# Performance work log

Hardware: AMD Instinct MI355X
Metric: run time of the kernel (lower is better)

## Reference

```python
import jax, jax.numpy as jnp
import numpy as np

B, S, D = 2, 2048, 4096
H, ROT = 16, 64
HD = D // H  # 256


def rotate_every_two(x):
    # x: (..., d) with d even; interleave (-x_odd, x_even)
    x1 = x[..., ::2]
    x2 = x[..., 1::2]
    return jnp.stack((-x2, x1), axis=-1).reshape(x.shape)


def setup_inputs() -> dict:
    key = jax.random.key(0)
    ks = jax.random.split(key, 8)
    hidden_states = jax.random.normal(ks[0], (B, S, D), dtype=jnp.float32)
    # GPT-J style repeat-interleaved sin/cos over rotary_dim, broadcast over heads
    inv_freq = 1.0 / (10000.0 ** (jnp.arange(0, ROT, 2, dtype=jnp.float32) / ROT))
    t = jnp.arange(S, dtype=jnp.float32)
    freqs = jnp.einsum('s,f->sf', t, inv_freq)                    # (S, ROT/2)
    freqs = jnp.repeat(freqs, 2, axis=-1)                         # (S, ROT)
    sin = jnp.sin(freqs)[None, :, None, :]                        # (1, S, 1, ROT)
    cos = jnp.cos(freqs)[None, :, None, :]
    scale = 0.02
    Wq = jax.random.normal(ks[1], (D, D), dtype=jnp.float32) * scale
    Wk = jax.random.normal(ks[2], (D, D), dtype=jnp.float32) * scale
    Wv = jax.random.normal(ks[3], (D, D), dtype=jnp.float32) * scale
    Wo = jax.random.normal(ks[4], (D, D), dtype=jnp.float32) * scale
    return {"hidden_states": hidden_states, "sin": sin, "cos": cos,
            "Wq": Wq, "Wk": Wk, "Wv": Wv, "Wo": Wo}


def reference(hidden_states, sin, cos, Wq, Wk, Wv, Wo):
    b, s, d = hidden_states.shape
    # projections (nn.Linear, no bias): y = x @ W.T
    q = (hidden_states @ Wq.T).reshape(b, s, H, HD)
    k = (hidden_states @ Wk.T).reshape(b, s, H, HD)
    v = (hidden_states @ Wv.T).reshape(b, s, H, HD)

    def rope(x):
        x_rot, x_pass = x[..., :ROT], x[..., ROT:]
        x_rot = x_rot * cos + rotate_every_two(x_rot) * sin
        return jnp.concatenate([x_rot, x_pass], axis=-1)

    q = rope(q).transpose(0, 2, 1, 3)  # (B, H, S, HD)
    k = rope(k).transpose(0, 2, 1, 3)
    v = v.transpose(0, 2, 1, 3)

    inv_scale = 1.0 / np.sqrt(HD).astype(np.float32)
    scores = jnp.einsum('bhqd,bhkd->bhqk', q, k) * inv_scale      # (B, H, S, S)
    # scaled_masked_triangular_softmax == causal masked softmax
    causal = jnp.tril(jnp.ones((s, s), dtype=bool))
    scores = jnp.where(causal[None, None], scores, jnp.finfo(scores.dtype).min)
    attn = jax.nn.softmax(scores, axis=-1)
    out = jnp.einsum('bhqk,bhkd->bhqd', attn, v)                  # (B, H, S, HD)
    out = out.transpose(0, 2, 1, 3).reshape(b, s, d)              # merge heads
    return out @ Wo.T
```

## Files before the change

kernel.cpp:

```cpp
#include <hip/hip_runtime.h>
#include <cstdint>
#include <cstddef>

#define TB 2
#define TS 2048
#define TD 4096
#define TH 16
#define THD 256
#define TROT 64
#define TM (TB*TS)

typedef __attribute__((ext_vector_type(8))) short bf16x8;
typedef __attribute__((ext_vector_type(4))) float f32x4;

#define LGKM0  asm volatile("s_waitcnt lgkmcnt(0)" ::: "memory")
#define VMCNT8 asm volatile("s_waitcnt vmcnt(8)" ::: "memory")
#define VMCNT4 asm volatile("s_waitcnt vmcnt(4)" ::: "memory")
#define VMCNT0 asm volatile("s_waitcnt vmcnt(0)" ::: "memory")
#define SBAR   __builtin_amdgcn_s_barrier()
#define SCHED0 __builtin_amdgcn_sched_barrier(0)
#define PRIO1  __builtin_amdgcn_s_setprio(1)
#define PRIO0  __builtin_amdgcn_s_setprio(0)

#if __has_builtin(__builtin_amdgcn_exp2f)
#define EXP2(x) __builtin_amdgcn_exp2f(x)
#else
#define EXP2(x) exp2f(x)
#endif

__device__ __forceinline__ unsigned short f2bf(float f) {
  union { float f; unsigned u; } v; v.f = f;
  return (unsigned short)((v.u + 0x7fffu + ((v.u >> 16) & 1u)) >> 16);
}

__device__ __forceinline__ void gld16(const void* g, void* l) {
  __builtin_amdgcn_global_load_lds(
      (const __attribute__((address_space(1))) unsigned int*)g,
      (__attribute__((address_space(3))) unsigned int*)l, 16, 0, 0);
}

__global__ __launch_bounds__(256) void k_cvt5(
    const float* __restrict__ s0, const float* __restrict__ s1,
    const float* __restrict__ s2, const float* __restrict__ s3,
    const float* __restrict__ s4, unsigned short* __restrict__ dst) {
  int i = blockIdx.x * 256 + threadIdx.x;
  int tsel = i >> 22, il = i & 4194303;
  const float* s = tsel == 0 ? s0 : tsel == 1 ? s1 : tsel == 2 ? s2 : tsel == 3 ? s3 : s4;
  float4 v = reinterpret_cast<const float4*>(s)[il];
  ushort4 o;
  o.x = f2bf(v.x); o.y = f2bf(v.y); o.z = f2bf(v.z); o.w = f2bf(v.w);
  *reinterpret_cast<ushort4*>(dst + (size_t)i * 4) = o;
}

#define GSTG(SBUF, SAB, SHALF, SKOFS) { \
    const unsigned short* _s = (SAB) ? srcB : srcA; \
    const int _b = (SBUF)*32768 + (SAB)*16384 + (SHALF)*8192; \
    gld16(_s + (size_t)(SHALF)*128*TD + (SKOFS) + roff[0], &lds[_b + t*8]); \
    gld16(_s + (size_t)(SHALF)*128*TD + (SKOFS) + roff[1], &lds[_b + (512+t)*8]); }

#define GLD_AF(DST, BUF, QA) { \
    _Pragma("unroll") for (int m = 0; m < 4; ++m) \
    _Pragma("unroll") for (int kk = 0; kk < 2; ++kk) \
      DST[m][kk] = *(const bf16x8*)&lds[(BUF)*32768 + (QA)*8192 + ((wm*4+m)*2+kk)*512 + llo]; }

#define GLD_BQ(DST, BUF, QB) { \
    _Pragma("unroll") for (int n = 0; n < 2; ++n) \
    _Pragma("unroll") for (int kk = 0; kk < 2; ++kk) \
      DST[n][kk] = *(const bf16x8*)&lds[(BUF)*32768 + 16384 + (QB)*8192 + ((wn*2+n)*2+kk)*512 + llo]; }

#define GMF(AF, BQ, QA, QB) { \
    _Pragma("unroll") for (int kk = 0; kk < 2; ++kk) \
    _Pragma("unroll") for (int m = 0; m < 4; ++m) \
    _Pragma("unroll") for (int n = 0; n < 2; ++n) \
      acc[QA][QB][m][n] = __builtin_amdgcn_mfma_f32_16x16x32_bf16( \
          AF[m][kk], BQ[n][kk], acc[QA][QB][m][n], 0,0,0); }

#define GEMM_MAIN_LOOP \
  GSTG(0,0,0, 0);  SCHED0; \
  GSTG(0,1,0, 0);  SCHED0; \
  GSTG(0,0,1, 0);  SCHED0; \
  GSTG(0,1,1, 0);  SCHED0; \
  GSTG(1,0,0, 64); SCHED0; \
  GSTG(1,1,0, 64); SCHED0; \
  VMCNT4; SBAR; SCHED0; \
  for (int i2 = 0; i2 < NT/2; ++i2) { \
    const int k1c = (2*i2+1) * 64; \
    const int k0n = (2*i2+2 < NT ? 2*i2+2 : NT-1) * 64; \
    const int k1n = (2*i2+3 < NT ? 2*i2+3 : NT-1) * 64; \
     \
    GLD_AF(afP, 0, 0); GLD_BQ(bqP, 0, 0); \
    GSTG(1,0,1, k1c); \
    LGKM0; SCHED0; \
    PRIO1; GLD_BQ(bqQ, 0, 1); GMF(afP, bqP, 0, 0); PRIO0; SCHED0; \
     \
    GSTG(1,1,1, k1c); \
    LGKM0; SCHED0; \
    PRIO1; GLD_AF(afQ, 0, 1); GMF(afP, bqQ, 0, 1); PRIO0; \
    SBAR; SCHED0; \
     \
    GSTG(0,0,0, k0n); \
    LGKM0; SCHED0; \
    PRIO1; GMF(afQ, bqP, 1, 0); PRIO0; SCHED0; \
     \
    GSTG(0,1,0, k0n); \
    VMCNT4; SBAR; \
    LGKM0; SCHED0; \
    PRIO1; GMF(afQ, bqQ, 1, 1); PRIO0; SCHED0; \
     \
    GLD_AF(afP, 1, 0); GLD_BQ(bqP, 1, 0); \
    GSTG(0,0,1, k0n); \
    LGKM0; SCHED0; \
    PRIO1; GLD_BQ(bqQ, 1, 1); GMF(afP, bqP, 0, 0); PRIO0; SCHED0; \
     \
    GSTG(0,1,1, k0n); \
    LGKM0; SCHED0; \
    PRIO1; GLD_AF(afQ, 1, 1); GMF(afP, bqQ, 0, 1); PRIO0; \
    SBAR; SCHED0; \
     \
    GSTG(1,0,0, k1n); \
    LGKM0; SCHED0; \
    PRIO1; GMF(afQ, bqP, 1, 0); PRIO0; SCHED0; \
     \
    GSTG(1,1,0, k1n); \
    VMCNT4; SBAR; \
    LGKM0; SCHED0; \
    PRIO1; GMF(afQ, bqQ, 1, 1); PRIO0; SCHED0; \
  }

#define GEMM_PREAMBLE \
  const int K = TD; \
  const int t = threadIdx.x; \
  const int w = t >> 6, l = t & 63, lr = l & 15, lh = l >> 4; \
  const int wm = w >> 2, wn = w & 3; \
  const int llo = lr * 32 + ((lh ^ ((lr >> 1) & 3)) * 8); \
  int roff[2]; \
  _Pragma("unroll") \
  for (int it = 0; it < 2; ++it) { \
    int c = it * 512 + t; \
    int rl = (c >> 2) & 15; \
    roff[it] = (16 * (c >> 7) + rl) * K + ((c >> 6) & 1) * 32 + ((c & 3) ^ ((rl >> 1) & 3)) * 8; \
  } \
  f32x4 acc[2][2][4][2]; \
  _Pragma("unroll") \
  for (int qa = 0; qa < 2; ++qa) \
  _Pragma("unroll") \
    for (int qb = 0; qb < 2; ++qb) \
  _Pragma("unroll") \
      for (int m = 0; m < 4; ++m) \
  _Pragma("unroll") \
        for (int n = 0; n < 2; ++n) acc[qa][qb][m][n] = 0.f; \
  bf16x8 afP[4][2], afQ[4][2], bqP[2][2], bqQ[2][2]; \
  const int NT = K / 64;

__global__ __launch_bounds__(512, 1) void k_gqkv(
    const unsigned short* __restrict__ A, const unsigned short* __restrict__ W,
    unsigned short* __restrict__ Qo, unsigned short* __restrict__ Ko,
    unsigned short* __restrict__ Vo,
    const float* __restrict__ sinp, const float* __restrict__ cosp)
{
  extern __shared__ unsigned short lds[];
  const int id = blockIdx.x;
  const int xcd = id & 7, kk_ = id >> 3;
  const int m0 = ((xcd & 1) * 8 + kk_ / 12) * 256;
  const int n0 = ((xcd >> 1) * 12 + kk_ % 12) * 256;

  GEMM_PREAMBLE
  const unsigned short* srcA = A + (size_t)m0 * K;
  const unsigned short* srcB = W + (size_t)n0 * K;

  GEMM_MAIN_LOOP

  VMCNT0;
  const int tsel = n0 >> 12;
  if (tsel == 2) {
    SBAR;
    const int n0v = n0 - 8192;
    const int b = m0 >> 11, sbase = m0 & (TS - 1);
#pragma unroll
    for (int qb = 0; qb < 2; ++qb)
#pragma unroll
      for (int n = 0; n < 2; ++n) {
        __syncthreads();
#pragma unroll
        for (int qa = 0; qa < 2; ++qa)
#pragma unroll
          for (int m = 0; m < 4; ++m) {
            int lcol = wn * 16 + lr;
            int srow = qa * 128 + wm * 64 + m * 16 + lh * 4;
            ushort4 o;
            o.x = f2bf(acc[qa][qb][m][n][0]); o.y = f2bf(acc[qa][qb][m][n][1]);
            o.z = f2bf(acc[qa][qb][m][n][2]); o.w = f2bf(acc[qa][qb][m][n][3]);
            *(ushort4*)&lds[lcol * 268 + srow] = o;
          }
        __syncthreads();
#pragma unroll
        for (int rr = 0; rr < 4; ++rr) {
          int idx = rr * 512 + t;
          int dl = idx >> 5, sc = (idx & 31) * 8;
          uint4 v = *(const uint4*)&lds[dl * 268 + sc];
          int d = n0v + qb * 128 + (dl >> 4) * 32 + n * 16 + (dl & 15);
          *(uint4*)(Vo + ((size_t)((b * TH + (d >> 8)) * THD + (d & 255))) * TS + sbase + sc) = v;
        }
      }
  } else {
    unsigned short* outp = tsel ? Ko : Qo;
    const int nbase = n0 & 4095;
#pragma unroll
    for (int qa = 0; qa < 2; ++qa)
#pragma unroll
      for (int qb = 0; qb < 2; ++qb)
#pragma unroll
        for (int m = 0; m < 4; ++m)
#pragma unroll
          for (int n = 0; n < 2; ++n)
#pragma unroll
            for (int r = 0; r < 4; ++r) {
              int row = m0 + qa * 128 + wm * 64 + m * 16 + lh * 4 + r;
              int col = nbase + qb * 128 + wn * 32 + n * 16 + lr;
              float x = acc[qa][qb][m][n][r];
              float part = __shfl_xor(x, 1, 64);
              int s = row & (TS - 1), b = row >> 11;
              int h = col >> 8, d = col & 255;
              float val = x;
              if (d < TROT) {
                float cc = cosp[s * TROT + d], ss = sinp[s * TROT + d];
                val = x * cc + ((d & 1) ? part : -part) * ss;
              }
              outp[((size_t)(b * TH + h) * TS + s) * THD + d] = f2bf(val);
            }
  }
}

__global__ __launch_bounds__(512, 1) void k_gout(
    const unsigned short* __restrict__ A, const unsigned short* __restrict__ W,
    float* __restrict__ out)
{
  extern __shared__ unsigned short lds[];
  const int id = blockIdx.x;
  const int xcd = id & 7, kk_ = id >> 3;
  const int m0 = ((xcd >> 1) * 4 + (kk_ >> 3)) * 256;
  const int n0 = ((xcd & 1) * 8 + (kk_ & 7)) * 256;

  GEMM_PREAMBLE
  const unsigned short* srcA = A + (size_t)m0 * K;
  const unsigned short* srcB = W + (size_t)n0 * K;

  GEMM_MAIN_LOOP

  VMCNT0;
#pragma unroll
  for (int qa = 0; qa < 2; ++qa)
#pragma unroll
    for (int qb = 0; qb < 2; ++qb)
#pragma unroll
      for (int m = 0; m < 4; ++m)
#pragma unroll
        for (int n = 0; n < 2; ++n)
#pragma unroll
          for (int r = 0; r < 4; ++r) {
            int row = m0 + qa * 128 + wm * 64 + m * 16 + lh * 4 + r;
            int col = n0 + qb * 128 + wn * 32 + n * 16 + lr;
            out[(size_t)row * TD + col] = acc[qa][qb][m][n][r];
          }
}

__global__ __launch_bounds__(256, 2) void k_fattn(
    const unsigned short* __restrict__ Qt, const unsigned short* __restrict__ Kt,
    const unsigned short* __restrict__ Vt, unsigned short* __restrict__ O)
{
  extern __shared__ unsigned short sh[];
  const int t = threadIdx.x, w = t >> 6, l = t & 63, lr = l & 15, lh = l >> 4;
  const int bh = blockIdx.x;
  const int qb = (gridDim.y - 1) - blockIdx.y;
  const int q0 = qb * 64;
  const int jmax = qb;
  const float SC = 0.0625f * 1.44269504f;

  const unsigned short* kbase = Kt + (size_t)bh * TS * THD;
  const unsigned short* vbase = Vt + (size_t)bh * THD * TS;

  const int llo = lr * 32 + ((lh ^ ((lr >> 1) & 3)) * 8);

  int koff[8], voff[8];
#pragma unroll
  for (int it = 0; it < 8; ++it) {
    int c = it * 256 + t;
    int row = (c >> 2) & 15;
    int scc = (c & 3) ^ ((row >> 1) & 3);
    koff[it] = (((c >> 9) & 3) * 16 + row) * THD + ((c >> 6) & 7) * 32 + scc * 8;
    voff[it] = (((c >> 6) & 15) * 16 + row) * TS + ((c >> 10) & 1) * 32 + scc * 8;
  }

  bf16x8 qf[8];
  const unsigned short* qp = Qt + ((size_t)bh * TS + q0 + w * 16 + lr) * THD;
#pragma unroll
  for (int kk = 0; kk < 8; ++kk) qf[kk] = *(const bf16x8*)(qp + kk * 32 + lh * 8);

  f32x4 oacc[16];
#pragma unroll
  for (int i = 0; i < 16; ++i) oacc[i] = 0.f;
  float mrow[4] = {-__builtin_inff(), -__builtin_inff(), -__builtin_inff(), -__builtin_inff()};
  float lrow[4] = {0.f, 0.f, 0.f, 0.f};

#pragma unroll
  for (int it = 0; it < 8; ++it) gld16(kbase + koff[it], &sh[(it*256 + t) * 8]);
#pragma unroll
  for (int it = 0; it < 8; ++it) gld16(vbase + voff[it], &sh[16384 + (it*256 + t) * 8]);

  for (int j = 0; j <= jmax; ++j) {
    const bool nx = (j < jmax);
    VMCNT8; SBAR; SCHED0;

    f32x4 sacc[4];
#pragma unroll
    for (int nt = 0; nt < 4; ++nt) sacc[nt] = 0.f;
    PRIO1;
#pragma unroll
    for (int kk = 0; kk < 8; ++kk)
#pragma unroll
      for (int nt = 0; nt < 4; ++nt) {
        bf16x8 kf = *(const bf16x8*)&sh[(nt*8 + kk)*512 + llo];
        sacc[nt] = __builtin_amdgcn_mfma_f32_16x16x32_bf16(qf[kk], kf, sacc[nt], 0, 0, 0);
      }
    PRIO0;
    LGKM0; SBAR; SCHED0;
    if (nx) {
      const unsigned short* kj = kbase + (size_t)(j + 1) * 64 * THD;
#pragma unroll
      for (int it = 0; it < 8; ++it) gld16(kj + koff[it], &sh[(it*256 + t) * 8]);
    }

    float p[4][4];
    const int qrow0 = q0 + w * 16 + lh * 4;
    if (j == jmax) {
#pragma unroll
      for (int nt = 0; nt < 4; ++nt) {
        int kpos = j * 64 + nt * 16 + lr;
#pragma unroll
        for (int r = 0; r < 4; ++r) {
          float sv = sacc[nt][r] * SC;
          if (kpos > qrow0 + r) sv = -__builtin_inff();
          p[nt][r] = sv;
        }
      }
    } else {
#pragma unroll
      for (int nt = 0; nt < 4; ++nt)
#pragma unroll
        for (int r = 0; r < 4; ++r)
          p[nt][r] = sacc[nt][r] * SC;
    }
    float lmax[4];
#pragma unroll
    for (int r = 0; r < 4; ++r)
      lmax[r] = fmaxf(fmaxf(p[0][r], p[1][r]), fmaxf(p[2][r], p[3][r]));
    float g = fmaxf(fmaxf(lmax[0] - mrow[0], lmax[1] - mrow[1]),
                    fmaxf(lmax[2] - mrow[2], lmax[3] - mrow[3]));
    if (__any(g > 11.5416f)) {
      float tmax[4] = {lmax[0], lmax[1], lmax[2], lmax[3]};
#pragma unroll
      for (int off = 1; off < 16; off <<= 1)
#pragma unroll
        for (int r = 0; r < 4; ++r) tmax[r] = fmaxf(tmax[r], __shfl_xor(tmax[r], off, 64));
      float alpha[4];
#pragma unroll
      for (int r = 0; r < 4; ++r) {
        float mn = fmaxf(mrow[r], tmax[r]);
        alpha[r] = EXP2(mrow[r] - mn);
        mrow[r] = mn;
        lrow[r] *= alpha[r];
      }
#pragma unroll
      for (int i = 0; i < 16; ++i)
#pragma unroll
        for (int r = 0; r < 4; ++r) oacc[i][r] *= alpha[r];
    }
#pragma unroll
    for (int r = 0; r < 4; ++r) {
      float pe0 = EXP2(p[0][r] - mrow[r]);
      float pe1 = EXP2(p[1][r] - mrow[r]);
      float pe2 = EXP2(p[2][r] - mrow[r]);
      float pe3 = EXP2(p[3][r] - mrow[r]);
      p[0][r] = pe0; p[1][r] = pe1; p[2][r] = pe2; p[3][r] = pe3;
      lrow[r] += (pe0 + pe1) + (pe2 + pe3);
    }

    const int wb = 32768 + w * 1152;
#pragma unroll
    for (int nt = 0; nt < 4; ++nt)
#pragma unroll
      for (int r = 0; r < 4; ++r)
        sh[wb + (lh*4 + r)*72 + nt*16 + lr] = f2bf(p[nt][r]);
    bf16x8 pfr0 = *(const bf16x8*)&sh[wb + lr*72 + lh*8];
    bf16x8 pfr1 = *(const bf16x8*)&sh[wb + lr*72 + 32 + lh*8];

    if (nx) { VMCNT8; } else { VMCNT0; }
    SBAR; SCHED0;
    PRIO1;
#pragma unroll
    for (int dt = 0; dt < 16; ++dt) {
      bf16x8 vf = *(const bf16x8*)&sh[16384 + dt*512 + llo];
      oacc[dt] = __builtin_amdgcn_mfma_f32_16x16x32_bf16(pfr0, vf, oacc[dt], 0, 0, 0);
    }
#pragma unroll
    for (int dt = 0; dt < 16; ++dt) {
      bf16x8 vf = *(const bf16x8*)&sh[16384 + (16 + dt)*512 + llo];
      oacc[dt] = __builtin_amdgcn_mfma_f32_16x16x32_bf16(pfr1, vf, oacc[dt], 0, 0, 0);
    }
    PRIO0;
    LGKM0; SBAR; SCHED0;
    if (nx) {
      const unsigned short* vj = vbase + (size_t)(j + 1) * 64;
#pragma unroll
      for (int it = 0; it < 8; ++it) gld16(vj + voff[it], &sh[16384 + (it*256 + t) * 8]);
    }
  }

#pragma unroll
  for (int off = 1; off < 16; off <<= 1)
#pragma unroll
    for (int r = 0; r < 4; ++r) lrow[r] += __shfl_xor(lrow[r], off, 64);

  const int b = bh >> 4, h = bh & 15;
  float inv[4];
#pragma unroll
  for (int r = 0; r < 4; ++r) inv[r] = 1.f / lrow[r];
#pragma unroll
  for (int dt = 0; dt < 16; ++dt)
#pragma unroll
    for (int r = 0; r < 4; ++r) {
      int s = q0 + w * 16 + lh * 4 + r;
      O[((size_t)(b * TS + s) * TH + h) * THD + dt * 16 + lr] = f2bf(oacc[dt][r] * inv[r]);
    }
}

extern "C" void kernel_launch(void* const* d_in, const int* in_sizes, int n_in,
                              void* d_out, int out_size, void* d_ws, size_t ws_size,
                              hipStream_t stream) {
  const float* hs   = (const float*)d_in[0];
  const float* sinp = (const float*)d_in[1];
  const float* cosp = (const float*)d_in[2];
  const float* Wq   = (const float*)d_in[3];
  const float* Wk   = (const float*)d_in[4];
  const float* Wv   = (const float*)d_in[5];
  const float* Wo   = (const float*)d_in[6];

  const size_t NE = (size_t)TM * TD;
  const size_t BYTES = NE * 2;
  char* ws = (char*)d_ws;
  unsigned short* hsb = (unsigned short*)(ws + 0*BYTES);
  unsigned short* Wqb = (unsigned short*)(ws + 1*BYTES);
  unsigned short* Wob = (unsigned short*)(ws + 4*BYTES);
  unsigned short* Qt  = (unsigned short*)(ws + 5*BYTES);
  unsigned short* Ktb = (unsigned short*)(ws + 6*BYTES);
  unsigned short* Vtb = (unsigned short*)(ws + 7*BYTES);
  unsigned short* Ob  = (unsigned short*)(ws + 8*BYTES);

  k_cvt5<<<81920, 256, 0, stream>>>(hs, Wq, Wk, Wv, Wo, hsb);

  k_gqkv<<<768, 512, 131072, stream>>>(hsb, Wqb, Qt, Ktb, Vtb, sinp, cosp);

  k_fattn<<<dim3(TB*TH, TS/64), 256, 74752, stream>>>(Qt, Ktb, Vtb, Ob);

  k_gout<<<256, 512, 131072, stream>>>(Ob, Wob, (float*)d_out);
}
```

Measured before the change: 672.5 us.

## Enlarge attention query tile to 128 rows with 8 waves sharing K/V tiles

The flash-attention kernel now handles 128 query rows per block with 512 threads (8 waves), so each K/V tile loaded into shared memory serves twice as many query rows and global K/V traffic halves. Query blocks are reordered so the longest causal rows launch first. Waves whose rows lie entirely above a key tile skip that tile's compute, and only tiles straddling the diagonal apply the mask. The P staging buffer now uses an XOR swizzle instead of padding. In exchange, idle waves wait at barriers on skipped tiles, and the grid drops to 512 blocks with more LDS per block, which may reduce occupancy and load balance.

```diff
diff --git a/kernel.cpp b/kernel.cpp
--- a/kernel.cpp
+++ b/kernel.cpp
@@ -264,16 +264,17 @@
           }
 }
 
-__global__ __launch_bounds__(256, 2) void k_fattn(
+__global__ __launch_bounds__(512, 2) void k_fattn(
     const unsigned short* __restrict__ Qt, const unsigned short* __restrict__ Kt,
     const unsigned short* __restrict__ Vt, unsigned short* __restrict__ O)
 {
   extern __shared__ unsigned short sh[];
   const int t = threadIdx.x, w = t >> 6, l = t & 63, lr = l & 15, lh = l >> 4;
   const int bh = blockIdx.x;
-  const int qb = (gridDim.y - 1) - blockIdx.y;
-  const int q0 = qb * 64;
-  const int jmax = qb;
+  const int y = blockIdx.y;
+  const int qb = (y < 8) ? (15 - y) : (y - 8);
+  const int q0 = qb * 128;
+  const int jmax = 2 * qb + 1;
   const float SC = 0.0625f * 1.44269504f;
 
   const unsigned short* kbase = Kt + (size_t)bh * TS * THD;
@@ -281,10 +282,10 @@
 
   const int llo = lr * 32 + ((lh ^ ((lr >> 1) & 3)) * 8);
 
-  int koff[8], voff[8];
-#pragma unroll
-  for (int it = 0; it < 8; ++it) {
-    int c = it * 256 + t;
+  int koff[4], voff[4];
+#pragma unroll
+  for (int it = 0; it < 4; ++it) {
+    int c = it * 512 + t;
     int row = (c >> 2) & 15;
     int scc = (c & 3) ^ ((row >> 1) & 3);
     koff[it] = (((c >> 9) & 3) * 16 + row) * THD + ((c >> 6) & 7) * 32 + scc * 8;
@@ -303,118 +304,133 @@
   float lrow[4] = {0.f, 0.f, 0.f, 0.f};
 
 #pragma unroll
-  for (int it = 0; it < 8; ++it) gld16(kbase + koff[it], &sh[(it*256 + t) * 8]);
-#pragma unroll
-  for (int it = 0; it < 8; ++it) gld16(vbase + voff[it], &sh[16384 + (it*256 + t) * 8]);
+  for (int it = 0; it < 4; ++it) gld16(kbase + koff[it], &sh[(it*512 + t) * 8]);
+#pragma unroll
+  for (int it = 0; it < 4; ++it) gld16(vbase + voff[it], &sh[16384 + (it*512 + t) * 8]);
+
+  const int qw = q0 + w * 16;
+  const int psb = 32768 + w * 1024;
 
   for (int j = 0; j <= jmax; ++j) {
     const bool nx = (j < jmax);
-    VMCNT8; SBAR; SCHED0;
+    const bool active = (j * 64) <= (qw + 15);
+    const bool diag   = (j * 64 + 63) > qw;
+    VMCNT4; SBAR; SCHED0;
 
     f32x4 sacc[4];
 #pragma unroll
     for (int nt = 0; nt < 4; ++nt) sacc[nt] = 0.f;
-    PRIO1;
-#pragma unroll
-    for (int kk = 0; kk < 8; ++kk)
-#pragma unroll
-      for (int nt = 0; nt < 4; ++nt) {
-        bf16x8 kf = *(const bf16x8*)&sh[(nt*8 + kk)*512 + llo];
-        sacc[nt] = __builtin_amdgcn_mfma_f32_16x16x32_bf16(qf[kk], kf, sacc[nt], 0, 0, 0);
-      }
-    PRIO0;
-    LGKM0; SBAR; SCHED0;
+    if (active) {
+      PRIO1;
+#pragma unroll
+      for (int kk = 0; kk < 8; ++kk)
+#pragma unroll
+        for (int nt = 0; nt < 4; ++nt) {
+          bf16x8 kf = *(const bf16x8*)&sh[(nt*8 + kk)*512 + llo];
+          sacc[nt] = __builtin_amdgcn_mfma_f32_16x16x32_bf16(qf[kk], kf, sacc[nt], 0, 0, 0);
+        }
+      PRIO0;
+      LGKM0;
+    }
+    SBAR; SCHED0;
     if (nx) {
       const unsigned short* kj = kbase + (size_t)(j + 1) * 64 * THD;
 #pragma unroll
-      for (int it = 0; it < 8; ++it) gld16(kj + koff[it], &sh[(it*256 + t) * 8]);
-    }
-
-    float p[4][4];
-    const int qrow0 = q0 + w * 16 + lh * 4;
-    if (j == jmax) {
-#pragma unroll
-      for (int nt = 0; nt < 4; ++nt) {
-        int kpos = j * 64 + nt * 16 + lr;
+      for (int it = 0; it < 4; ++it) gld16(kj + koff[it], &sh[(it*512 + t) * 8]);
+    }
+
+    if (active) {
+      float p[4][4];
+      const int qrow0 = qw + lh * 4;
+      if (diag) {
+#pragma unroll
+        for (int nt = 0; nt < 4; ++nt) {
+          int kpos = j * 64 + nt * 16 + lr;
+#pragma unroll
+          for (int r = 0; r < 4; ++r) {
+            float sv = sacc[nt][r] * SC;
+            if (kpos > qrow0 + r) sv = -__builtin_inff();
+            p[nt][r] = sv;
+          }
+        }
+      } else {
+#pragma unroll
+        for (int nt = 0; nt < 4; ++nt)
+#pragma unroll
+          for (int r = 0; r < 4; ++r)
+            p[nt][r] = sacc[nt][r] * SC;
+      }
+      float lmax[4];
+#pragma unroll
+      for (int r = 0; r < 4; ++r)
+        lmax[r] = fmaxf(fmaxf(p[0][r], p[1][r]), fmaxf(p[2][r], p[3][r]));
+      float g = fmaxf(fmaxf(lmax[0] - mrow[0], lmax[1] - mrow[1]),
+                      fmaxf(lmax[2] - mrow[2], lmax[3] - mrow[3]));
+      if (__any(g > 11.5416f)) {
+        float tmax[4] = {lmax[0], lmax[1], lmax[2], lmax[3]};
+#pragma unroll
+        for (int off = 1; off < 16; off <<= 1)
+#pragma unroll
+          for (int r = 0; r < 4; ++r) tmax[r] = fmaxf(tmax[r], __shfl_xor(tmax[r], off, 64));
+        float alpha[4];
 #pragma unroll
         for (int r = 0; r < 4; ++r) {
-          float sv = sacc[nt][r] * SC;
-          if (kpos > qrow0 + r) sv = -__builtin_inff();
-          p[nt][r] = sv;
+          float mn = fmaxf(mrow[r], tmax[r]);
+          alpha[r] = EXP2(mrow[r] - mn);
+          mrow[r] = mn;
+          lrow[r] *= alpha[r];
         }
-      }
-    } else {
+#pragma unroll
+        for (int i = 0; i < 16; ++i)
+#pragma unroll
+          for (int r = 0; r < 4; ++r) oacc[i][r] *= alpha[r];
+      }
+#pragma unroll
+      for (int r = 0; r < 4; ++r) {
+        float pe0 = EXP2(p[0][r] - mrow[r]);
+        float pe1 = EXP2(p[1][r] - mrow[r]);
+        float pe2 = EXP2(p[2][r] - mrow[r]);
+        float pe3 = EXP2(p[3][r] - mrow[r]);
+        p[0][r] = pe0; p[1][r] = pe1; p[2][r] = pe2; p[3][r] = pe3;
+        lrow[r] += (pe0 + pe1) + (pe2 + pe3);
+      }
+
 #pragma unroll
       for (int nt = 0; nt < 4; ++nt)
 #pragma unroll
-        for (int r = 0; r < 4; ++r)
-          p[nt][r] = sacc[nt][r] * SC;
-    }
-    float lmax[4];
-#pragma unroll
-    for (int r = 0; r < 4; ++r)
-      lmax[r] = fmaxf(fmaxf(p[0][r], p[1][r]), fmaxf(p[2][r], p[3][r]));
-    float g = fmaxf(fmaxf(lmax[0] - mrow[0], lmax[1] - mrow[1]),
-                    fmaxf(lmax[2] - mrow[2], lmax[3] - mrow[3]));
-    if (__any(g > 11.5416f)) {
-      float tmax[4] = {lmax[0], lmax[1], lmax[2], lmax[3]};
-#pragma unroll
-      for (int off = 1; off < 16; off <<= 1)
-#pragma unroll
-        for (int r = 0; r < 4; ++r) tmax[r] = fmaxf(tmax[r], __shfl_xor(tmax[r], off, 64));
-      float alpha[4];
-#pragma unroll
-      for (int r = 0; r < 4; ++r) {
-        float mn = fmaxf(mrow[r], tmax[r]);
-        alpha[r] = EXP2(mrow[r] - mn);
-        mrow[r] = mn;
-        lrow[r] *= alpha[r];
-      }
-#pragma unroll
-      for (int i = 0; i < 16; ++i)
-#pragma unroll
-        for (int r = 0; r < 4; ++r) oacc[i][r] *= alpha[r];
-    }
-#pragma unroll
-    for (int r = 0; r < 4; ++r) {
-      float pe0 = EXP2(p[0][r] - mrow[r]);
-      float pe1 = EXP2(p[1][r] - mrow[r]);
-      float pe2 = EXP2(p[2][r] - mrow[r]);
-      float pe3 = EXP2(p[3][r] - mrow[r]);
-      p[0][r] = pe0; p[1][r] = pe1; p[2][r] = pe2; p[3][r] = pe3;
-      lrow[r] += (pe0 + pe1) + (pe2 + pe3);
-    }
-
-    const int wb = 32768 + w * 1152;
-#pragma unroll
-    for (int nt = 0; nt < 4; ++nt)
-#pragma unroll
-      for (int r = 0; r < 4; ++r)
-        sh[wb + (lh*4 + r)*72 + nt*16 + lr] = f2bf(p[nt][r]);
-    bf16x8 pfr0 = *(const bf16x8*)&sh[wb + lr*72 + lh*8];
-    bf16x8 pfr1 = *(const bf16x8*)&sh[wb + lr*72 + 32 + lh*8];
-
-    if (nx) { VMCNT8; } else { VMCNT0; }
+        for (int r = 0; r < 4; ++r) {
+          int row = lh * 4 + r;
+          sh[psb + row * 64 + ((nt * 16 + lr) ^ ((row & 7) * 8))] = f2bf(p[nt][r]);
+        }
+    }
+
+    VMCNT4;
     SBAR; SCHED0;
-    PRIO1;
-#pragma unroll
-    for (int dt = 0; dt < 16; ++dt) {
-      bf16x8 vf = *(const bf16x8*)&sh[16384 + dt*512 + llo];
-      oacc[dt] = __builtin_amdgcn_mfma_f32_16x16x32_bf16(pfr0, vf, oacc[dt], 0, 0, 0);
-    }
-#pragma unroll
-    for (int dt = 0; dt < 16; ++dt) {
-      bf16x8 vf = *(const bf16x8*)&sh[16384 + (16 + dt)*512 + llo];
-      oacc[dt] = __builtin_amdgcn_mfma_f32_16x16x32_bf16(pfr1, vf, oacc[dt], 0, 0, 0);
-    }
-    PRIO0;
-    LGKM0; SBAR; SCHED0;
+    if (active) {
+      bf16x8 pfr0 = *(const bf16x8*)&sh[psb + lr * 64 + ((lh * 8) ^ ((lr & 7) * 8))];
+      bf16x8 pfr1 = *(const bf16x8*)&sh[psb + lr * 64 + (((32 + lh * 8)) ^ ((lr & 7) * 8))];
+      PRIO1;
+#pragma unroll
+      for (int dt = 0; dt < 16; ++dt) {
+        bf16x8 vf = *(const bf16x8*)&sh[16384 + dt*512 + llo];
+        oacc[dt] = __builtin_amdgcn_mfma_f32_16x16x32_bf16(pfr0, vf, oacc[dt], 0, 0, 0);
+      }
+#pragma unroll
+      for (int dt = 0; dt < 16; ++dt) {
+        bf16x8 vf = *(const bf16x8*)&sh[16384 + (16 + dt)*512 + llo];
+        oacc[dt] = __builtin_amdgcn_mfma_f32_16x16x32_bf16(pfr1, vf, oacc[dt], 0, 0, 0);
+      }
+      PRIO0;
+      LGKM0;
+    }
+    SBAR; SCHED0;
     if (nx) {
       const unsigned short* vj = vbase + (size_t)(j + 1) * 64;
 #pragma unroll
-      for (int it = 0; it < 8; ++it) gld16(vj + voff[it], &sh[16384 + (it*256 + t) * 8]);
+      for (int it = 0; it < 4; ++it) gld16(vj + voff[it], &sh[16384 + (it*512 + t) * 8]);
     }
   }
+  VMCNT0;
 
 #pragma unroll
   for (int off = 1; off < 16; off <<= 1)
@@ -460,7 +476,7 @@
 
   k_gqkv<<<768, 512, 131072, stream>>>(hsb, Wqb, Qt, Ktb, Vtb, sinp, cosp);
 
-  k_fattn<<<dim3(TB*TH, TS/64), 256, 74752, stream>>>(Qt, Ktb, Vtb, Ob);
+  k_fattn<<<dim3(TB*TH, 16), 512, 81920, stream>>>(Qt, Ktb, Vtb, Ob);
 
   k_gout<<<256, 512, 131072, stream>>>(Ob, Wob, (float*)d_out);
 }
```

Result: slower. 690.1 us (+2.6%).
